# Performance work log

Hardware: AMD Instinct MI355X
Metric: run time of the kernel (lower is better)

The kernel has to match this reference:

```python
import jax, jax.numpy as jnp
import numpy as np

B, S, HID = 2, 2048, 2048
NH, NG = 32, 8
HD = HID // NH  # 64
KV = HD * NG    # 512


def setup_inputs() -> dict:
    key = jax.random.key(0)
    ks = jax.random.split(key, 9)
    w = lambda k, shp: jax.random.normal(k, shp, dtype=jnp.float32) * 0.02
    return {
        "hidden_state": jax.random.normal(ks[0], (B, S, HID), dtype=jnp.float32),
        "Wq": w(ks[1], (HID, HID)), "bq": jnp.zeros((HID,), jnp.float32),
        "Wk": w(ks[2], (HID, KV)),  "bk": jnp.zeros((KV,), jnp.float32),
        "Wv": w(ks[3], (HID, KV)),  "bv": jnp.zeros((KV,), jnp.float32),
        "Wo": w(ks[4], (HID, HID)), "bo": jnp.zeros((HID,), jnp.float32),
    }


def reference(hidden_state, Wq, bq, Wk, bk, Wv, bv, Wo, bo):
    bs, seq, _ = hidden_state.shape
    rep = NH // NG  # heads per KV group

    q = hidden_state @ Wq + bq                      # [B,S,HID]
    k = hidden_state @ Wk + bk                      # [B,S,KV]
    v = hidden_state @ Wv + bv

    q = q.reshape(bs, seq, NH, HD).transpose(0, 2, 1, 3)   # [B,NH,S,D]
    k = k.reshape(bs, seq, NG, HD).transpose(0, 2, 1, 3)   # [B,NG,S,D]
    v = v.reshape(bs, seq, NG, HD).transpose(0, 2, 1, 3)
    # grouped-KV expansion: each group repeated consecutively rep times
    k = jnp.repeat(k, rep, axis=1)                          # [B,NH,S,D]
    v = jnp.repeat(v, rep, axis=1)

    scores = jnp.einsum("bhqd,bhkd->bhqk", q, k) / jnp.sqrt(jnp.float32(HD))
    probs = jax.nn.softmax(scores, axis=-1)
    out = jnp.einsum("bhqk,bhkd->bhqd", probs, v)           # [B,NH,S,D]
    out = out.transpose(0, 2, 1, 3).reshape(bs, seq, HID)
    return out @ Wo + bo
```

## Files before the change

### kernel.cpp

```cpp
#include <hip/hip_runtime.h>
#include <hip/hip_bf16.h>
#include <math.h>

typedef __bf16 bf16x8 __attribute__((ext_vector_type(8)));
typedef float f32x4 __attribute__((ext_vector_type(4)));
typedef __hip_bfloat16 bf16_t;

#define MFMA_BF16(a, b, c) __builtin_amdgcn_mfma_f32_16x16x32_bf16((a), (b), (c), 0, 0, 0)

__device__ __forceinline__ void async_copy16(const bf16_t* g, bf16_t* lds_base) {
  __builtin_amdgcn_global_load_lds(
      (const __attribute__((address_space(1))) unsigned int*)g,
      (__attribute__((address_space(3))) unsigned int*)lds_base,
      16, 0, 0);
}

__device__ __forceinline__ unsigned fbits(float x) { return __builtin_bit_cast(unsigned, x); }

__global__ __launch_bounds__(256) void prep(
    const float* __restrict__ hidden, const float* __restrict__ Wq, const float* __restrict__ Wk,
    const float* __restrict__ Wv, const float* __restrict__ Wo,
    const float* __restrict__ bq, const float* __restrict__ bk, const float* __restrict__ bv,
    bf16_t* __restrict__ hiddenB, bf16_t* __restrict__ WqkvT, bf16_t* __restrict__ WoT,
    float* __restrict__ bqkv, float c1) {
  __shared__ float tile[64][65];
  int bid = blockIdx.x;
  const int t = threadIdx.x;
  if (bid < 8192) {
    const int i = bid * 256 + t;
    float4 v = ((const float4*)hidden)[i];
    union { bf16_t h[4]; ushort4 u; } cv;
    cv.h[0] = __float2bfloat16(v.x);
    cv.h[1] = __float2bfloat16(v.y);
    cv.h[2] = __float2bfloat16(v.z);
    cv.h[3] = __float2bfloat16(v.w);
    ((ushort4*)hiddenB)[i] = cv.u;
    return;
  }
  bid -= 8192;
  if (bid >= 2560) {
    const int i = (bid - 2560) * 256 + t;
    float v;
    if (i < 2048) v = bq[i] * c1;
    else if (i < 2560) v = bk[i - 2048];
    else v = bv[i - 2560];
    bqkv[i] = v;
    return;
  }
  const float* src;
  bf16_t* dst;
  int Cc, bx, by;
  float scale = 1.0f;
  if (bid < 1024) { src = Wq; dst = WqkvT; Cc = 2048; bx = bid & 31; by = bid >> 5; scale = c1; }
  else if (bid < 1280) { bid -= 1024; src = Wk; dst = WqkvT + (size_t)2048 * 2048; Cc = 512; bx = bid & 7; by = bid >> 3; }
  else if (bid < 1536) { bid -= 1280; src = Wv; dst = WqkvT + (size_t)2560 * 2048; Cc = 512; bx = bid & 7; by = bid >> 3; }
  else { bid -= 1536; src = Wo; dst = WoT; Cc = 2048; bx = bid & 31; by = bid >> 5; }
  const int tx = t & 63, ty = t >> 6;
  const int c0 = bx * 64, r0 = by * 64;
#pragma unroll
  for (int i = ty; i < 64; i += 4)
    tile[i][tx] = src[(size_t)(r0 + i) * Cc + c0 + tx];
  __syncthreads();
#pragma unroll
  for (int i = ty; i < 64; i += 4)
    dst[(size_t)(c0 + i) * 2048 + r0 + tx] = __float2bfloat16(tile[tx][i] * scale);
}

template <typename TOUT>
__global__ __launch_bounds__(256, 3) void gemm_bt(
    const bf16_t* __restrict__ A, const bf16_t* __restrict__ Bt,
    const float* __restrict__ bias, TOUT* __restrict__ C, bf16_t* __restrict__ vTp,
    int M, int N, int K) {
  __shared__ alignas(16) bf16_t As[128 * 64];
  __shared__ alignas(16) bf16_t Bs[128 * 64];

  const int tid = threadIdx.x;
  const int w = tid >> 6, lane = tid & 63;
  const int quad = lane >> 4, l16 = lane & 15;
  const int wm = w >> 1, wn = w & 1;
  const int m0 = blockIdx.y * 128, n0 = blockIdx.x * 128;

  f32x4 acc[4][4] = {};

  const int rr = lane >> 3;
  const int scol = ((lane & 7) ^ rr) * 8;
  const int sx = l16 & 7;

  for (int k0 = 0; k0 < K; k0 += 64) {
    __syncthreads();
#pragma unroll
    for (int c = 0; c < 4; ++c) {
      const int r = w * 32 + c * 8 + rr;
      async_copy16(A + (size_t)(m0 + r) * K + k0 + scol, &As[(w * 32 + c * 8) * 64]);
      async_copy16(Bt + (size_t)(n0 + r) * K + k0 + scol, &Bs[(w * 32 + c * 8) * 64]);
    }
    __syncthreads();

#pragma unroll
    for (int kh = 0; kh < 2; ++kh) {
      bf16x8 af[4], bf[4];
#pragma unroll
      for (int i = 0; i < 4; ++i) {
        af[i] = *(const bf16x8*)&As[(wm * 64 + i * 16 + l16) * 64 + (((kh * 4 + quad) ^ sx) * 8)];
        bf[i] = *(const bf16x8*)&Bs[(wn * 64 + i * 16 + l16) * 64 + (((kh * 4 + quad) ^ sx) * 8)];
      }
#pragma unroll
      for (int i = 0; i < 4; ++i)
#pragma unroll
        for (int j = 0; j < 4; ++j)
          acc[i][j] = MFMA_BF16(af[i], bf[j], acc[i][j]);
    }
  }

  if (vTp != nullptr && n0 >= 2560) {
#pragma unroll
    for (int i = 0; i < 4; ++i) {
      const int row = m0 + wm * 64 + i * 16 + quad * 4;
      const int bb = row >> 11, s = row & 2047;
#pragma unroll
      for (int j = 0; j < 4; ++j) {
        const int col = n0 + wn * 64 + j * 16 + l16;
        const float bv = bias[col];
        union { bf16_t h[4]; ushort4 u; } cv;
#pragma unroll
        for (int r = 0; r < 4; ++r) cv.h[r] = __float2bfloat16(acc[i][j][r] + bv);
        *(ushort4*)&vTp[((size_t)bb * 512 + (col - 2560)) * 2048 + s] = cv.u;
      }
    }
    return;
  }

#pragma unroll
  for (int i = 0; i < 4; ++i) {
    const int row = m0 + wm * 64 + i * 16 + quad * 4;
#pragma unroll
    for (int j = 0; j < 4; ++j) {
      const int col = n0 + wn * 64 + j * 16 + l16;
      const float bv = bias[col];
#pragma unroll
      for (int r = 0; r < 4; ++r) {
        const float val = acc[i][j][r] + bv;
        if constexpr (__is_same(TOUT, float)) {
          C[(size_t)(row + r) * N + col] = val;
        } else {
          C[(size_t)(row + r) * N + col] = __float2bfloat16(val);
        }
      }
    }
  }
}

__global__ __launch_bounds__(512, 2) void gemm256(
    const bf16_t* __restrict__ A, const bf16_t* __restrict__ Bt,
    const float* __restrict__ bias, bf16_t* __restrict__ C, bf16_t* __restrict__ vTp) {
  constexpr int N = 3072, K = 2048;
  __shared__ alignas(16) bf16_t As[2 * 256 * 64];
  __shared__ alignas(16) bf16_t Bs[2 * 256 * 64];

  const int tid = threadIdx.x;
  const int w = tid >> 6, lane = tid & 63;
  const int quad = lane >> 4, l16 = lane & 15;
  const int wm = w >> 2, wn = w & 3;

  const int flat = blockIdx.y * 12 + blockIdx.x;
  const int swz = (flat & 7) * 24 + (flat >> 3);
  const int m0 = (swz / 12) * 256, n0 = (swz % 12) * 256;

  const int rr = lane >> 3, c7 = lane & 7;
  const int scol = (c7 ^ rr) * 8;
  const int sx = l16 & 7;

  auto stA = [&](int t, int h) {
    const int kb = (t & 31) * 64;
    const int rbase = h * 128 + w * 8;
    bf16_t* d0 = &As[(t & 1) * (256 * 64) + rbase * 64];
    const bf16_t* s0 = A + (size_t)(m0 + rbase + rr) * K + kb + scol;
    async_copy16(s0, d0);
    async_copy16(s0 + (size_t)64 * K, d0 + 64 * 64);
  };
  auto stB = [&](int t, int h) {
    const int kb = (t & 31) * 64;
    const int rbase = h * 128 + w * 8;
    bf16_t* d0 = &Bs[(t & 1) * (256 * 64) + rbase * 64];
    const bf16_t* s0 = Bt + (size_t)(n0 + rbase + rr) * K + kb + scol;
    async_copy16(s0, d0);
    async_copy16(s0 + (size_t)64 * K, d0 + 64 * 64);
  };

  f32x4 acc[4][2][4] = {};

  stB(0, 0); stB(0, 1); stA(0, 0); stA(0, 1);
  stB(1, 0); stB(1, 1);
  asm volatile("s_waitcnt vmcnt(4)" ::: "memory");
  __builtin_amdgcn_s_barrier();
  __builtin_amdgcn_sched_barrier(0);

  for (int it = 0; it < 16; ++it) {
#pragma unroll
    for (int kg = 0; kg < 2; ++kg) {
      const int t = it * 2 + kg;
      const int ta = (t + 1) & 31;
      const int tb = (t + 2) & 31;
      const bf16_t* Asb = &As[(t & 1) * (256 * 64)];
      const bf16_t* Bsb = &Bs[(t & 1) * (256 * 64)];

      bf16x8 b[4][2];
#pragma unroll
      for (int ni = 0; ni < 4; ++ni)
#pragma unroll
        for (int kk = 0; kk < 2; ++kk)
          b[ni][kk] = *(const bf16x8*)&Bsb[(wn * 64 + ni * 16 + l16) * 64 +
                                           (((kk * 4 + quad) ^ sx) * 8)];
      bf16x8 a01[2][2][2];
#pragma unroll
      for (int p = 0; p < 2; ++p)
#pragma unroll
        for (int mi = 0; mi < 2; ++mi)
#pragma unroll
          for (int kk = 0; kk < 2; ++kk)
            a01[p][mi][kk] = *(const bf16x8*)&Asb[(wm * 128 + p * 32 + mi * 16 + l16) * 64 +
                                                  (((kk * 4 + quad) ^ sx) * 8)];
      stA(ta, 0); stA(ta, 1);
      __builtin_amdgcn_s_barrier();
      __builtin_amdgcn_s_setprio(1);
#pragma unroll
      for (int p = 0; p < 2; ++p)
#pragma unroll
        for (int kk = 0; kk < 2; ++kk)
#pragma unroll
          for (int mi = 0; mi < 2; ++mi)
#pragma unroll
            for (int ni = 0; ni < 4; ++ni)
              acc[p][mi][ni] = MFMA_BF16(a01[p][mi][kk], b[ni][kk], acc[p][mi][ni]);
      __builtin_amdgcn_s_setprio(0);
      __builtin_amdgcn_s_barrier();

      bf16x8 a23[2][2][2];
#pragma unroll
      for (int p = 0; p < 2; ++p)
#pragma unroll
        for (int mi = 0; mi < 2; ++mi)
#pragma unroll
          for (int kk = 0; kk < 2; ++kk)
            a23[p][mi][kk] = *(const bf16x8*)&Asb[(wm * 128 + (p + 2) * 32 + mi * 16 + l16) * 64 +
                                                  (((kk * 4 + quad) ^ sx) * 8)];
      stB(tb, 0); stB(tb, 1);
      __builtin_amdgcn_s_barrier();
      __builtin_amdgcn_s_setprio(1);
#pragma unroll
      for (int p = 0; p < 2; ++p)
#pragma unroll
        for (int kk = 0; kk < 2; ++kk)
#pragma unroll
          for (int mi = 0; mi < 2; ++mi)
#pragma unroll
            for (int ni = 0; ni < 4; ++ni)
              acc[p + 2][mi][ni] = MFMA_BF16(a23[p][mi][kk], b[ni][kk], acc[p + 2][mi][ni]);
      __builtin_amdgcn_s_setprio(0);
      asm volatile("s_waitcnt vmcnt(4)" ::: "memory");
      __builtin_amdgcn_s_barrier();
      __builtin_amdgcn_sched_barrier(0);
    }
  }

  asm volatile("s_waitcnt vmcnt(0)" ::: "memory");

  if (n0 >= 2560) {
#pragma unroll
    for (int p = 0; p < 4; ++p)
#pragma unroll
      for (int mi = 0; mi < 2; ++mi) {
        const int row4 = m0 + wm * 128 + p * 32 + mi * 16 + quad * 4;
        const int bb = row4 >> 11, s = row4 & 2047;
#pragma unroll
        for (int ni = 0; ni < 4; ++ni) {
          const int col = n0 + wn * 64 + ni * 16 + l16;
          const float bv = bias[col];
          union { bf16_t h[4]; ushort4 u; } cv;
#pragma unroll
          for (int r = 0; r < 4; ++r) cv.h[r] = __float2bfloat16(acc[p][mi][ni][r] + bv);
          *(ushort4*)&vTp[((size_t)bb * 512 + (col - 2560)) * 2048 + s] = cv.u;
        }
      }
    return;
  }

#pragma unroll
  for (int p = 0; p < 4; ++p)
#pragma unroll
    for (int mi = 0; mi < 2; ++mi) {
      const int row4 = m0 + wm * 128 + p * 32 + mi * 16 + quad * 4;
#pragma unroll
      for (int ni = 0; ni < 4; ++ni) {
        const int col = n0 + wn * 64 + ni * 16 + l16;
        const float bv = bias[col];
#pragma unroll
        for (int r = 0; r < 4; ++r)
          C[(size_t)(row4 + r) * N + col] = __float2bfloat16(acc[p][mi][ni][r] + bv);
      }
    }
}

__global__ __launch_bounds__(256, 4) void gqa_attn(
    const bf16_t* __restrict__ QKV, const bf16_t* __restrict__ VT, bf16_t* __restrict__ O,
    int xoff) {
  constexpr int S = 2048, HID = 2048, QKVS = 3072, HD = 64;
  const int tid = threadIdx.x;
  const int w = tid >> 6, lane = tid & 63;
  const int quad = lane >> 4, l16 = lane & 15;
  const int hp = blockIdx.y, b = blockIdx.z;
  const int h = hp * 2 + (w & 1);
  const int g = hp >> 1;
  const int q0 = (xoff + blockIdx.x) * 64 + (w >> 1) * 32;

  __shared__ alignas(16) bf16_t Ks[64 * 64];
  __shared__ alignas(16) bf16_t VTs[64 * 64];
  __shared__ alignas(16) bf16_t Ps[128 * 64];

  bf16x8 qf[2][2];
#pragma unroll
  for (int mt = 0; mt < 2; ++mt)
#pragma unroll
    for (int ks = 0; ks < 2; ++ks)
      qf[mt][ks] = *(const bf16x8*)&QKV[(size_t)(b * S + q0 + mt * 16 + l16) * QKVS +
                                        h * HD + ks * 32 + quad * 8];

  const int rr = lane >> 3, c7 = lane & 7;
  const int sx = l16 & 7;

  const bf16_t* Kbase = QKV + (size_t)b * S * QKVS + 2048 + g * HD;
  const bf16_t* Vbase = VT + (size_t)(b * 512 + g * HD) * S;

  const int srow = w * 16 + rr;
  const bf16_t* kp0 = Kbase + (size_t)srow * QKVS + c7 * 8;
  const bf16_t* kp1 = kp0 + (size_t)8 * QKVS;
  const bf16_t* vp0 = Vbase + (size_t)srow * S + c7 * 8;
  const bf16_t* vp1 = vp0 + (size_t)8 * S;
  bf16_t* KsW0 = &Ks[(srow)*64 + (c7 ^ rr) * 8];
  bf16_t* KsW1 = KsW0 + 8 * 64;
  bf16_t* VsW0 = &VTs[(srow)*64 + (c7 ^ rr) * 8];
  bf16_t* VsW1 = VsW0 + 8 * 64;

  f32x4 oacc[2][4] = {};
  f32x4 lacc[2] = {};
  bf16x8 ones;
#pragma unroll
  for (int j = 0; j < 8; ++j) ones[j] = (__bf16)1.0f;

  uint4 kr0 = *(const uint4*)kp0;
  uint4 kr1 = *(const uint4*)kp1;
  uint4 vr0 = *(const uint4*)vp0;
  uint4 vr1 = *(const uint4*)vp1;

  for (int s0 = 0; s0 < S; s0 += 64) {
    __syncthreads();
    *(uint4*)KsW0 = kr0;
    *(uint4*)KsW1 = kr1;
    *(uint4*)VsW0 = vr0;
    *(uint4*)VsW1 = vr1;
    const int sn = (s0 + 64) & (S - 1);
    kr0 = *(const uint4*)(kp0 + (size_t)sn * QKVS);
    kr1 = *(const uint4*)(kp1 + (size_t)sn * QKVS);
    vr0 = *(const uint4*)(vp0 + sn);
    vr1 = *(const uint4*)(vp1 + sn);
    __syncthreads();

    __builtin_amdgcn_s_setprio(1);
#pragma unroll
    for (int nt = 0; nt < 4; ++nt) {
      bf16x8 kf0 = *(const bf16x8*)&Ks[(nt * 16 + l16) * 64 + ((quad ^ sx) * 8)];
      bf16x8 kf1 = *(const bf16x8*)&Ks[(nt * 16 + l16) * 64 + (((4 + quad) ^ sx) * 8)];
#pragma unroll
      for (int mt = 0; mt < 2; ++mt) {
        f32x4 s = {};
        s = MFMA_BF16(kf0, qf[mt][0], s);
        s = MFMA_BF16(kf1, qf[mt][1], s);
        const float p0 = __builtin_amdgcn_exp2f(s[0]);
        const float p1 = __builtin_amdgcn_exp2f(s[1]);
        const float p2 = __builtin_amdgcn_exp2f(s[2]);
        const float p3 = __builtin_amdgcn_exp2f(s[3]);
        uint2 pk;
        pk.x = __builtin_amdgcn_perm(fbits(p1), fbits(p0), 0x07060302);
        pk.y = __builtin_amdgcn_perm(fbits(p3), fbits(p2), 0x07060302);
        *(uint2*)&Ps[(w * 32 + mt * 16 + l16) * 64 +
                     (((nt * 2 + (quad >> 1)) ^ sx) * 8) + (quad & 1) * 4] = pk;
      }
    }

#pragma unroll
    for (int kc = 0; kc < 2; ++kc) {
      bf16x8 pf[2];
#pragma unroll
      for (int mt = 0; mt < 2; ++mt) {
        pf[mt] = *(const bf16x8*)&Ps[(w * 32 + mt * 16 + l16) * 64 + (((kc * 4 + quad) ^ sx) * 8)];
        lacc[mt] = MFMA_BF16(pf[mt], ones, lacc[mt]);
      }
#pragma unroll
      for (int dt = 0; dt < 4; ++dt) {
        bf16x8 vf = *(const bf16x8*)&VTs[(dt * 16 + l16) * 64 + (((kc * 4 + quad) ^ sx) * 8)];
#pragma unroll
        for (int mt = 0; mt < 2; ++mt)
          oacc[mt][dt] = MFMA_BF16(pf[mt], vf, oacc[mt][dt]);
      }
    }
    __builtin_amdgcn_s_setprio(0);
  }

#pragma unroll
  for (int mt = 0; mt < 2; ++mt) {
    float linv[4];
#pragma unroll
    for (int r = 0; r < 4; ++r) linv[r] = 1.0f / lacc[mt][r];
#pragma unroll
    for (int dt = 0; dt < 4; ++dt)
#pragma unroll
      for (int r = 0; r < 4; ++r)
        O[(size_t)(b * S + q0 + mt * 16 + quad * 4 + r) * HID + h * HD + dt * 16 + l16] =
            __float2bfloat16(oacc[mt][dt][r] * linv[r]);
  }
}

extern "C" void kernel_launch(void* const* d_in, const int* in_sizes, int n_in,
                              void* d_out, int out_size, void* d_ws, size_t ws_size,
                              hipStream_t stream) {
  const float* hidden = (const float*)d_in[0];
  const float* Wq = (const float*)d_in[1];
  const float* bq = (const float*)d_in[2];
  const float* Wk = (const float*)d_in[3];
  const float* bk = (const float*)d_in[4];
  const float* Wv = (const float*)d_in[5];
  const float* bv = (const float*)d_in[6];
  const float* Wo = (const float*)d_in[7];
  const float* bo = (const float*)d_in[8];
  float* out = (float*)d_out;

  constexpr int B = 2, S = 2048, HID = 2048, KV = 512, QKVN = 3072;
  constexpr int M = B * S;
  const float c1 = 0.125f * 1.44269504089f;

  char* ws = (char*)d_ws;
  bf16_t* hiddenB = (bf16_t*)ws; ws += (size_t)M * HID * 2;
  bf16_t* WqkvT = (bf16_t*)ws;   ws += (size_t)QKVN * HID * 2;
  bf16_t* WoT = (bf16_t*)ws;     ws += (size_t)HID * HID * 2;
  bf16_t* qkv = (bf16_t*)ws;     ws += (size_t)M * QKVN * 2;
  bf16_t* vT = (bf16_t*)ws;      ws += (size_t)M * KV * 2;
  bf16_t* attn = (bf16_t*)ws;    ws += (size_t)M * HID * 2;
  float* bqkv = (float*)ws;      ws += QKVN * 4;

  prep<<<8192 + 2560 + 12, 256, 0, stream>>>(hidden, Wq, Wk, Wv, Wo, bq, bk, bv,
                                             hiddenB, WqkvT, WoT, bqkv, c1);

  gemm256<<<dim3(QKVN / 256, M / 256), 512, 0, stream>>>(hiddenB, WqkvT, bqkv, qkv, vT);

  gqa_attn<<<dim3(S / 64, 16, B), 256, 0, stream>>>(qkv, vT, attn, 0);

  gemm_bt<float><<<dim3(HID / 128, M / 128), 256, 0, stream>>>(
      attn, WoT, bo, out, (bf16_t*)nullptr, M, HID, HID);
}
```

Before: 311.2 us.

## Share K/V tiles across all four heads of a group and double-buffer LDS

The attention block grows from 256 to 512 threads, so one block covers all four query heads of a KV group instead of two. Each K/V tile is therefore loaded once per group rather than twice, halving global K/V traffic. The LDS K/V buffers are double-buffered, which removes one of the two __syncthreads per iteration. In exchange LDS use per block doubles and the launch bounds change from (256,4) to (512,2), which may limit occupancy.

```diff
diff --git a/kernel.cpp b/kernel.cpp
--- a/kernel.cpp
+++ b/kernel.cpp
@@ -301,21 +301,19 @@
     }
 }
 
-__global__ __launch_bounds__(256, 4) void gqa_attn(
-    const bf16_t* __restrict__ QKV, const bf16_t* __restrict__ VT, bf16_t* __restrict__ O,
-    int xoff) {
+__global__ __launch_bounds__(512, 2) void gqa_attn(
+    const bf16_t* __restrict__ QKV, const bf16_t* __restrict__ VT, bf16_t* __restrict__ O) {
   constexpr int S = 2048, HID = 2048, QKVS = 3072, HD = 64;
   const int tid = threadIdx.x;
   const int w = tid >> 6, lane = tid & 63;
   const int quad = lane >> 4, l16 = lane & 15;
-  const int hp = blockIdx.y, b = blockIdx.z;
-  const int h = hp * 2 + (w & 1);
-  const int g = hp >> 1;
-  const int q0 = (xoff + blockIdx.x) * 64 + (w >> 1) * 32;
-
-  __shared__ alignas(16) bf16_t Ks[64 * 64];
-  __shared__ alignas(16) bf16_t VTs[64 * 64];
-  __shared__ alignas(16) bf16_t Ps[128 * 64];
+  const int g = blockIdx.y, b = blockIdx.z;
+  const int h = g * 4 + (w & 3);
+  const int q0 = blockIdx.x * 64 + (w >> 2) * 32;
+
+  __shared__ alignas(16) bf16_t Ks[2 * 64 * 64];
+  __shared__ alignas(16) bf16_t VTs[2 * 64 * 64];
+  __shared__ alignas(16) bf16_t Ps[256 * 64];
 
   bf16x8 qf[2][2];
 #pragma unroll
@@ -331,15 +329,10 @@
   const bf16_t* Kbase = QKV + (size_t)b * S * QKVS + 2048 + g * HD;
   const bf16_t* Vbase = VT + (size_t)(b * 512 + g * HD) * S;
 
-  const int srow = w * 16 + rr;
-  const bf16_t* kp0 = Kbase + (size_t)srow * QKVS + c7 * 8;
-  const bf16_t* kp1 = kp0 + (size_t)8 * QKVS;
-  const bf16_t* vp0 = Vbase + (size_t)srow * S + c7 * 8;
-  const bf16_t* vp1 = vp0 + (size_t)8 * S;
-  bf16_t* KsW0 = &Ks[(srow)*64 + (c7 ^ rr) * 8];
-  bf16_t* KsW1 = KsW0 + 8 * 64;
-  bf16_t* VsW0 = &VTs[(srow)*64 + (c7 ^ rr) * 8];
-  bf16_t* VsW1 = VsW0 + 8 * 64;
+  const int srow = w * 8 + rr;
+  const bf16_t* kp = Kbase + (size_t)srow * QKVS + c7 * 8;
+  const bf16_t* vp = Vbase + (size_t)srow * S + c7 * 8;
+  const int woff = srow * 64 + (c7 ^ rr) * 8;
 
   f32x4 oacc[2][4] = {};
   f32x4 lacc[2] = {};
@@ -347,29 +340,23 @@
 #pragma unroll
   for (int j = 0; j < 8; ++j) ones[j] = (__bf16)1.0f;
 
-  uint4 kr0 = *(const uint4*)kp0;
-  uint4 kr1 = *(const uint4*)kp1;
-  uint4 vr0 = *(const uint4*)vp0;
-  uint4 vr1 = *(const uint4*)vp1;
-
-  for (int s0 = 0; s0 < S; s0 += 64) {
+  uint4 kr = *(const uint4*)kp;
+  uint4 vr = *(const uint4*)vp;
+
+  for (int it = 0; it < 32; ++it) {
+    const int cur = (it & 1) * (64 * 64);
+    *(uint4*)&Ks[cur + woff] = kr;
+    *(uint4*)&VTs[cur + woff] = vr;
+    const int sn = ((it + 1) & 31) * 64;
+    kr = *(const uint4*)(kp + (size_t)sn * QKVS);
+    vr = *(const uint4*)(vp + sn);
     __syncthreads();
-    *(uint4*)KsW0 = kr0;
-    *(uint4*)KsW1 = kr1;
-    *(uint4*)VsW0 = vr0;
-    *(uint4*)VsW1 = vr1;
-    const int sn = (s0 + 64) & (S - 1);
-    kr0 = *(const uint4*)(kp0 + (size_t)sn * QKVS);
-    kr1 = *(const uint4*)(kp1 + (size_t)sn * QKVS);
-    vr0 = *(const uint4*)(vp0 + sn);
-    vr1 = *(const uint4*)(vp1 + sn);
-    __syncthreads();
 
     __builtin_amdgcn_s_setprio(1);
 #pragma unroll
     for (int nt = 0; nt < 4; ++nt) {
-      bf16x8 kf0 = *(const bf16x8*)&Ks[(nt * 16 + l16) * 64 + ((quad ^ sx) * 8)];
-      bf16x8 kf1 = *(const bf16x8*)&Ks[(nt * 16 + l16) * 64 + (((4 + quad) ^ sx) * 8)];
+      bf16x8 kf0 = *(const bf16x8*)&Ks[cur + (nt * 16 + l16) * 64 + ((quad ^ sx) * 8)];
+      bf16x8 kf1 = *(const bf16x8*)&Ks[cur + (nt * 16 + l16) * 64 + (((4 + quad) ^ sx) * 8)];
 #pragma unroll
       for (int mt = 0; mt < 2; ++mt) {
         f32x4 s = {};
@@ -397,7 +384,7 @@
       }
 #pragma unroll
       for (int dt = 0; dt < 4; ++dt) {
-        bf16x8 vf = *(const bf16x8*)&VTs[(dt * 16 + l16) * 64 + (((kc * 4 + quad) ^ sx) * 8)];
+        bf16x8 vf = *(const bf16x8*)&VTs[cur + (dt * 16 + l16) * 64 + (((kc * 4 + quad) ^ sx) * 8)];
 #pragma unroll
         for (int mt = 0; mt < 2; ++mt)
           oacc[mt][dt] = MFMA_BF16(pf[mt], vf, oacc[mt][dt]);
@@ -452,7 +439,7 @@
 
   gemm256<<<dim3(QKVN / 256, M / 256), 512, 0, stream>>>(hiddenB, WqkvT, bqkv, qkv, vT);
 
-  gqa_attn<<<dim3(S / 64, 16, B), 256, 0, stream>>>(qkv, vT, attn, 0);
+  gqa_attn<<<dim3(S / 64, 8, B), 512, 0, stream>>>(qkv, vT, attn);
 
   gemm_bt<float><<<dim3(HID / 128, M / 128), 256, 0, stream>>>(
       attn, WoT, bo, out, (bf16_t*)nullptr, M, HID, HID);
```

New measurement: 302.3 us. -2.9%, faster.
